# Kernel tuning notes

Measured on AMD Instinct MI355X. Metric: run time of the kernel, lower is better.

## Reference

```python
import jax, jax.numpy as jnp
import numpy as np

T, N_SAT, G_SAT, HID, IN = 256, 1024, 2048, 256, 32

def _make_sids(key):
    # per-timestep unique visible-satellite ids (matches dict-keyed state, no dup scatter)
    keys = jax.random.split(key, T)
    return jax.vmap(lambda k: jax.random.permutation(k, G_SAT)[:N_SAT])(keys).astype(jnp.int32)

def setup_inputs() -> dict:
    key = jax.random.key(0)
    ks = jax.random.split(key, 16)
    s = 0.05
    return {
        "x_rec": jax.random.normal(ks[0], (T, 1, IN), jnp.float32),
        "x_sat": jax.random.normal(ks[1], (T, N_SAT, IN), jnp.float32),
        "y_true": jax.random.normal(ks[2], (1, 2), jnp.float32),
        "W_rec": jax.random.normal(ks[3], (4, IN, HID), jnp.float32) * s,
        "b_rec": jax.random.normal(ks[4], (4, HID), jnp.float32) * s,
        "W_sat": jax.random.normal(ks[5], (4, IN, HID), jnp.float32) * s,
        "b_sat": jax.random.normal(ks[6], (4, HID), jnp.float32) * s,
        "s2r_lw": jax.random.normal(ks[7], (4, HID, HID), jnp.float32) * s,
        "s2r_lb": jax.random.normal(ks[8], (4, HID), jnp.float32) * s,
        "s2r_rw": jax.random.normal(ks[9], (4, HID, HID), jnp.float32) * s,
        "r2s_lw": jax.random.normal(ks[10], (4, HID, HID), jnp.float32) * s,
        "r2s_lb": jax.random.normal(ks[11], (4, HID), jnp.float32) * s,
        "r2s_rw": jax.random.normal(ks[12], (4, HID, HID), jnp.float32) * s,
        "W_out": jax.random.normal(ks[13], (HID, 2), jnp.float32) * s,
        "b_out": jax.random.normal(ks[14], (2,), jnp.float32) * s,
        "s_ids": _make_sids(ks[15]),
    }

def _gates(pre):
    # pre: [4, ..., HID] in gate order (i, f, c, o)
    return (jax.nn.sigmoid(pre[0]), jax.nn.sigmoid(pre[1]),
            jnp.tanh(pre[2]), jax.nn.sigmoid(pre[3]))

def reference(x_rec, x_sat, y_true, W_rec, b_rec, W_sat, b_sat,
              s2r_lw, s2r_lb, s2r_rw, r2s_lw, r2s_lb, r2s_rw,
              W_out, b_out, s_ids):
    hid = W_out.shape[0]

    def step(carry, inp):
        h_rec, c_rec, Hg, Cg = carry          # h_rec/c_rec: [hid]; Hg/Cg: [G, hid]
        xr, xs, sid = inp                      # xr: [1, in]; xs: [N, in]; sid: [N]
        h_sat = Hg[sid]                        # gather visible satellite states [N, hid]
        c_sat = Cg[sid]
        # per-gate input projections
        xr_p = jnp.einsum('i,gio->go', xr[0], W_rec) + b_rec          # [4, hid]
        xs_p = jnp.einsum('ni,gio->gno', xs, W_sat) + b_sat[:, None]  # [4, N, hid]
        # SAGEConv sat->rec: mean over all visible sats (star topology)
        mean_sat = jnp.mean(h_sat, axis=0)                            # [hid]
        conv_rec = (jnp.einsum('h,gho->go', mean_sat, s2r_lw) + s2r_lb
                    + jnp.einsum('h,gho->go', h_rec, s2r_rw))         # [4, hid]
        # SAGEConv rec->sat: each sat's sole neighbor is the receiver
        conv_sat = ((jnp.einsum('h,gho->go', h_rec, r2s_lw) + r2s_lb)[:, None, :]
                    + jnp.einsum('nh,gho->gno', h_sat, r2s_rw))       # [4, N, hid]
        i_r, f_r, t_r, o_r = _gates(xr_p + conv_rec)
        c_rec_n = f_r * c_rec + i_r * t_r
        h_rec_n = o_r * jnp.tanh(c_rec_n)
        i_s, f_s, t_s, o_s = _gates(xs_p + conv_sat)
        c_sat_n = f_s * c_sat + i_s * t_s
        h_sat_n = o_s * jnp.tanh(c_sat_n)
        Hg = Hg.at[sid].set(h_sat_n)
        Cg = Cg.at[sid].set(c_sat_n)
        return (h_rec_n, c_rec_n, Hg, Cg), None

    init = (jnp.zeros((hid,), x_rec.dtype), jnp.zeros((hid,), x_rec.dtype),
            jnp.zeros((G_SAT, hid), x_rec.dtype), jnp.zeros((G_SAT, hid), x_rec.dtype))
    (h_rec, _, _, _), _ = jax.lax.scan(step, init, (x_rec, x_sat, s_ids))
    pred = h_rec[None, :] @ W_out + b_out   # dropout is identity in eval mode
    return pred, y_true
```

## Files before the change

kernel.cpp:

```cpp
#include <hip/hip_runtime.h>
#include <cstddef>

#define T_STEPS  256
#define NSAT     1024
#define GSAT     2048
#define HID      256
#define IN_DIM   32
#define KTOT     288

typedef short  s16x8 __attribute__((ext_vector_type(8)));
typedef short  s16x4 __attribute__((ext_vector_type(4)));
typedef float  f32x4 __attribute__((ext_vector_type(4)));
typedef unsigned short ushort_t;

__device__ inline ushort_t f2bf(float f) {
    unsigned u = __builtin_bit_cast(unsigned, f);
    u += 0x7fffu + ((u >> 16) & 1u);
    return (ushort_t)(u >> 16);
}
__device__ inline float bf2f(ushort_t h) {
    unsigned u = ((unsigned)h) << 16;
    return __builtin_bit_cast(float, u);
}
__device__ inline float sigm(float x) { return 1.f / (1.f + __expf(-x)); }
__device__ inline float tanh_(float x) {
    float a = fabsf(x);
    float e = __expf(-2.f * a);
    float r = (1.f - e) / (1.f + e);
    return copysignf(r, x);
}

__global__ void k_zero(float* p, size_t n) {
    size_t i = (size_t)blockIdx.x * blockDim.x + threadIdx.x;
    size_t stride = (size_t)gridDim.x * blockDim.x;
    for (; i < n; i += stride) p[i] = 0.f;
}

__global__ void k_bconv(const float* __restrict__ r2s_rw,
                        const float* __restrict__ W_sat,
                        ushort_t* __restrict__ BsatT) {
    int c = blockIdx.x;
    int g = (c >> 3) & 3, o = (c >> 5) * 8 + (c & 7);
    for (int k = threadIdx.x; k < KTOT; k += 256) {
        float v = (k < 256) ? r2s_rw[((size_t)g * 256 + k) * 256 + o]
                            : W_sat[((size_t)g * 32 + (k - 256)) * 256 + o];
        BsatT[(size_t)c * KTOT + k] = f2bf(v);
    }
}

__global__ void k_rlw(const float* __restrict__ r2s_lw, ushort_t* __restrict__ rlw_bf) {
    int c = blockIdx.x;
    int g = (c >> 3) & 3, o = (c >> 5) * 8 + (c & 7);
    int h = threadIdx.x;
    rlw_bf[(size_t)c * 256 + h] = f2bf(r2s_lw[((size_t)g * 256 + h) * 256 + o]);
}

__global__ void k_biasC(const float* __restrict__ r2s_lb, const float* __restrict__ b_sat,
                        float* __restrict__ biasC) {
    int c = blockIdx.x * 256 + threadIdx.x;
    if (c < 1024) {
        int g = (c >> 3) & 3, o = (c >> 5) * 8 + (c & 7);
        biasC[c] = r2s_lb[g * 256 + o] + b_sat[g * 256 + o];
    }
}

__global__ void k_inv(const int* __restrict__ s_ids, ushort_t* __restrict__ pos_inv) {
    int t = blockIdx.x;
    for (int n = threadIdx.x; n < NSAT; n += 256)
        pos_inv[(size_t)t * GSAT + s_ids[(size_t)t * NSAT + n]] = (ushort_t)(n + 1);
}

__global__ void k_asrc(const int* __restrict__ s_ids, const ushort_t* __restrict__ pos_inv,
                       int* __restrict__ asrc) {
    int t = blockIdx.x;
    for (int n = threadIdx.x; n < NSAT; n += 256) {
        int j = s_ids[(size_t)t * NSAT + n];
        int e = 1024 + j;
        if (t > 0) {
            int p = (int)pos_inv[(size_t)(t - 1) * GSAT + j] - 1;
            if (p >= 0) e = p;
        }
        asrc[(size_t)t * NSAT + n] = e;
    }
}

__global__ void k_bits(const int* __restrict__ s_ids, const ushort_t* __restrict__ pos_inv,
                       unsigned* __restrict__ nxt_bits) {
    int t = blockIdx.x, w = threadIdx.x;
    unsigned bits = 0;
    if (t + 1 < T_STEPS) {
        for (int i = 0; i < 32; i++) {
            int j = s_ids[(size_t)t * NSAT + w * 32 + i];
            if (pos_inv[(size_t)(t + 1) * GSAT + j] > 0) bits |= (1u << i);
        }
    }
    nxt_bits[t * 32 + w] = bits;
}

__global__ void k_old(const int* __restrict__ s_ids, const ushort_t* __restrict__ pos_inv,
                      short* __restrict__ old_src, int* __restrict__ old_cnt) {
    int t = blockIdx.x;
    if (t + 1 >= T_STEPS) return;
    for (int n = threadIdx.x; n < NSAT; n += 256) {
        int j = s_ids[(size_t)(t + 1) * NSAT + n];
        if (pos_inv[(size_t)t * GSAT + j] == 0) {
            int slot = atomicAdd(&old_cnt[t], 1);
            short e = (short)(-(j + 1));
            if (t > 0) {
                int p = (int)pos_inv[(size_t)(t - 1) * GSAT + j] - 1;
                if (p >= 0) e = (short)p;
            }
            old_src[(size_t)t * NSAT + slot] = e;
        }
    }
}

__global__ void k_lv(const int* __restrict__ s_ids, const ushort_t* __restrict__ pos_inv,
                     int* __restrict__ lv, int* __restrict__ lv_cnt) {
    int t = blockIdx.x;
    if (t == 0) return;
    for (int n = threadIdx.x; n < NSAT; n += 256) {
        int j = s_ids[(size_t)(t - 1) * NSAT + n];
        if (pos_inv[(size_t)t * GSAT + j] == 0) {
            int slot = atomicAdd(&lv_cnt[t], 1);
            lv[(size_t)t * NSAT + slot] = (n << 16) | j;
        }
    }
}

__global__ void k_wtb(const float* __restrict__ in, ushort_t* __restrict__ outT) {
    __shared__ float tl[32][33];
    int g = blockIdx.z;
    int h0 = blockIdx.x * 32, o0 = blockIdx.y * 32;
    int lx = threadIdx.x & 31, ly = threadIdx.x >> 5;
#pragma unroll
    for (int i = 0; i < 32; i += 8)
        tl[ly + i][lx] = in[((size_t)g * 256 + h0 + ly + i) * 256 + o0 + lx];
    __syncthreads();
#pragma unroll
    for (int i = 0; i < 32; i += 8)
        outT[((size_t)g * 256 + o0 + ly + i) * 256 + h0 + lx] = f2bf(tl[lx][ly + i]);
}

__global__ void k_wrt(const float* __restrict__ W_rec, float* __restrict__ W_recT) {
    int idx = blockIdx.x * 256 + threadIdx.x;
    int g = idx >> 8, o = idx & 255;
#pragma unroll
    for (int i = 0; i < 32; i++)
        W_recT[(size_t)idx * 32 + i] = W_rec[((size_t)g * 32 + i) * 256 + o];
}

__launch_bounds__(256)
__global__ void k_step(int t,
    const float* __restrict__ x_rec, const float* __restrict__ x_sat,
    const float* __restrict__ b_rec, const float* __restrict__ s2r_lb,
    const int* __restrict__ asrc, const unsigned* __restrict__ nxt_bits,
    const short* __restrict__ old_src, const int* __restrict__ old_cnt,
    const int* __restrict__ lv, const int* __restrict__ lv_cnt,
    const ushort_t* __restrict__ BsatT, const ushort_t* __restrict__ rlw_bf,
    const float* __restrict__ biasC,
    const ushort_t* __restrict__ s2r_rwT, const ushort_t* __restrict__ s2r_lwT,
    const float* __restrict__ W_recT,
    float* __restrict__ meanN,
    float* __restrict__ oldpart,
    float* __restrict__ crec,
    float* __restrict__ pre_rec,
    ushort_t* __restrict__ Hg_bf, ushort_t* __restrict__ Cg_bf,
    const ushort_t* __restrict__ HnP, ushort_t* __restrict__ HnC,
    const ushort_t* __restrict__ CnP, ushort_t* __restrict__ CnC)
{
    const int b = blockIdx.x, tid = threadIdx.x;
    const float* preP  = pre_rec + ((t + 1) & 1) * 1024;
    const float* crecP = crec + (t & 1) * 256;

    if (b < 256) {
        const int by = b >> 5, bxc = b & 31;
        __shared__ ushort_t hr_bfs[256];
        __shared__ float    bias_s[32];
        __shared__ float    rl_s[32];
        __shared__ float    pre_s[128][33];

        const int w = tid >> 6, l = tid & 63;
        const int lr = l & 15, kb = (l >> 4) * 8;
        const int r0 = w * 32 + lr, r1 = r0 + 16;
        const int* asrc_t = asrc + (size_t)t * NSAT + by * 128;

        const int e0 = asrc_t[r0], e1 = asrc_t[r1];
        if (tid < 32) bias_s[tid] = biasC[bxc * 32 + tid];
        const int n_ep = tid >> 1, oi0_ep = (tid & 1) * 4;
        const int og0_ep = bxc * 8 + oi0_ep;
        const int en_ep = asrc_t[n_ep];
        const ushort_t* csrc = (en_ep < 1024) ? CnP + (size_t)en_ep * HID + og0_ep
                                              : Cg_bf + (size_t)(en_ep - 1024) * HID + og0_ep;
        s16x4 cold4 = *(const s16x4*)csrc;
        const int lv_m = lv_cnt[t];
        ushort_t pH[4], pC[4]; int pJ[4];
#pragma unroll
        for (int i = 0; i < 4; i++) {
            int k = b + i * 256;
            if (k < lv_m) {
                int pv = lv[(size_t)t * NSAT + k];
                int pos = pv >> 16; pJ[i] = pv & 0xffff;
                pH[i] = HnP[(size_t)pos * HID + tid];
                pC[i] = CnP[(size_t)pos * HID + tid];
            } else pJ[i] = -1;
        }
        {
            float h = 0.f;
            if (t > 0) {
                float pi = preP[tid], pf = preP[256 + tid], pc = preP[512 + tid], po = preP[768 + tid];
                float cp = (t >= 2) ? crecP[tid] : 0.f;
                float cn = sigm(pf) * cp + sigm(pi) * tanh_(pc);
                h = sigm(po) * tanh_(cn);
            }
            hr_bfs[tid] = f2bf(h);
        }

        const ushort_t* a0 = (e0 < 1024) ? HnP + (size_t)e0 * HID : Hg_bf + (size_t)(e0 - 1024) * HID;
        const ushort_t* a1 = (e1 < 1024) ? HnP + (size_t)e1 * HID : Hg_bf + (size_t)(e1 - 1024) * HID;
        const ushort_t* bp0 = BsatT + ((size_t)(bxc * 32 + lr)) * KTOT;
        const ushort_t* bp1 = bp0 + (size_t)16 * KTOT;
        f32x4 a00 = {0.f,0.f,0.f,0.f}, a01 = a00, a10 = a00, a11 = a00;
#pragma unroll
        for (int kc = 0; kc < 8; kc++) {
            int k0 = kc * 32 + kb;
            s16x8 af0 = *(const s16x8*)(a0 + k0);
            s16x8 af1 = *(const s16x8*)(a1 + k0);
            s16x8 bv0 = *(const s16x8*)(bp0 + k0);
            s16x8 bv1 = *(const s16x8*)(bp1 + k0);
            a00 = __builtin_amdgcn_mfma_f32_16x16x32_bf16(af0, bv0, a00, 0, 0, 0);
            a01 = __builtin_amdgcn_mfma_f32_16x16x32_bf16(af0, bv1, a01, 0, 0, 0);
            a10 = __builtin_amdgcn_mfma_f32_16x16x32_bf16(af1, bv0, a10, 0, 0, 0);
            a11 = __builtin_amdgcn_mfma_f32_16x16x32_bf16(af1, bv1, a11, 0, 0, 0);
        }
        {
            const float* ax0 = x_sat + ((size_t)t * NSAT + by * 128 + r0) * IN_DIM + kb;
            const float* ax1 = x_sat + ((size_t)t * NSAT + by * 128 + r1) * IN_DIM + kb;
            f32x4 x00 = *(const f32x4*)ax0, x01 = *(const f32x4*)(ax0 + 4);
            f32x4 x10 = *(const f32x4*)ax1, x11 = *(const f32x4*)(ax1 + 4);
            s16x8 af0, af1;
#pragma unroll
            for (int e = 0; e < 4; e++) {
                af0[e] = (short)f2bf(x00[e]); af0[4 + e] = (short)f2bf(x01[e]);
                af1[e] = (short)f2bf(x10[e]); af1[4 + e] = (short)f2bf(x11[e]);
            }
            int k0 = 256 + kb;
            s16x8 bv0 = *(const s16x8*)(bp0 + k0);
            s16x8 bv1 = *(const s16x8*)(bp1 + k0);
            a00 = __builtin_amdgcn_mfma_f32_16x16x32_bf16(af0, bv0, a00, 0, 0, 0);
            a01 = __builtin_amdgcn_mfma_f32_16x16x32_bf16(af0, bv1, a01, 0, 0, 0);
            a10 = __builtin_amdgcn_mfma_f32_16x16x32_bf16(af1, bv0, a10, 0, 0, 0);
            a11 = __builtin_amdgcn_mfma_f32_16x16x32_bf16(af1, bv1, a11, 0, 0, 0);
        }
#pragma unroll
        for (int rr = 0; rr < 4; rr++) {
            int ro = (l >> 4) * 4 + rr;
            pre_s[w * 32 + ro][lr]           = a00[rr];
            pre_s[w * 32 + ro][16 + lr]      = a01[rr];
            pre_s[w * 32 + 16 + ro][lr]      = a10[rr];
            pre_s[w * 32 + 16 + ro][16 + lr] = a11[rr];
        }
        __syncthreads();

        {
            int c = tid >> 3, sub = tid & 7;
            const ushort_t* wp = rlw_bf + ((size_t)(bxc * 32 + c)) * 256 + sub * 32;
            float acc = 0.f;
#pragma unroll
            for (int q = 0; q < 4; q++) {
                s16x8 wv = *(const s16x8*)(wp + q * 8);
#pragma unroll
                for (int e = 0; e < 8; e++)
                    acc += bf2f(hr_bfs[sub * 32 + q * 8 + e]) * bf2f((ushort_t)wv[e]);
            }
            acc += __shfl_down(acc, 4);
            acc += __shfl_down(acc, 2);
            acc += __shfl_down(acc, 1);
            if (sub == 0) rl_s[c] = acc + bias_s[c];
        }
        __syncthreads();

        {
            int n = n_ep, oi0 = oi0_ep, og0 = og0_ep;
            int gr = by * 128 + n;
            bool nxt = (t + 1 < T_STEPS) && ((nxt_bits[t * 32 + (gr >> 5)] >> (gr & 31)) & 1u);
            f32x4 hf; s16x4 cnew, hnew;
#pragma unroll
            for (int e = 0; e < 4; e++) {
                int oi = oi0 + e;
                float pi = pre_s[n][oi]      + rl_s[oi];
                float pf = pre_s[n][8 + oi]  + rl_s[8 + oi];
                float pc = pre_s[n][16 + oi] + rl_s[16 + oi];
                float po = pre_s[n][24 + oi] + rl_s[24 + oi];
                float ig = sigm(pi), fg = sigm(pf), tg = tanh_(pc), oo = sigm(po);
                float cn = fg * bf2f((ushort_t)cold4[e]) + ig * tg;
                float hn = oo * tanh_(cn);
                hf[e] = hn;
                cnew[e] = (short)f2bf(cn);
                hnew[e] = (short)f2bf(hn);
            }
            *(s16x4*)(CnC + (size_t)gr * HID + og0) = cnew;
            *(s16x4*)(HnC + (size_t)gr * HID + og0) = hnew;
#pragma unroll
            for (int e = 0; e < 4; e++) pre_s[n][oi0 + e] = nxt ? hf[e] : 0.f;
        }
        __syncthreads();
        if (t + 1 < T_STEPS && tid < 8) {
            float s = 0.f;
            for (int n = 0; n < 128; n++) s += pre_s[n][tid];
            meanN[((t + 1) & 1) * 2048 + by * 256 + bxc * 8 + tid] = s;
        }

#pragma unroll
        for (int i = 0; i < 4; i++) {
            if (pJ[i] >= 0) {
                Hg_bf[(size_t)pJ[i] * HID + tid] = pH[i];
                Cg_bf[(size_t)pJ[i] * HID + tid] = pC[i];
            }
        }
    } else {
        const int r = b - 256;
        __shared__ float mean_s[256], hr_s[256], xr_s[32];
        const int m_old = (t + 1 < T_STEPS) ? old_cnt[t] : 0;
        {
            float s = 0.f;
            const float* mp = meanN + (t & 1) * 2048;
#pragma unroll
            for (int p = 0; p < 8; p++) s += mp[p * 256 + tid];
            const float* op = oldpart + (t & 1) * 8192;
#pragma unroll 8
            for (int p = 0; p < 32; p++) s += op[p * 256 + tid];
            mean_s[tid] = s * (1.f / 1024.f);
        }
        {
            float h = 0.f, cn = 0.f;
            if (t > 0) {
                float pi = preP[tid], pf = preP[256 + tid], pc = preP[512 + tid], po = preP[768 + tid];
                float cp = (t >= 2) ? crecP[tid] : 0.f;
                cn = sigm(pf) * cp + sigm(pi) * tanh_(pc);
                h = sigm(po) * tanh_(cn);
            }
            hr_s[tid] = h;
            if (r == 0 && t > 0) crec[((t + 1) & 1) * 256 + tid] = cn;
        }
        if (tid < 32) xr_s[tid] = x_rec[(size_t)t * IN_DIM + tid];
        __syncthreads();
        float s_old = 0.f;
        {
            const short* osp = old_src + (size_t)t * NSAT;
#pragma unroll 2
            for (int k = r; k < m_old; k += 32) {
                int e = osp[k];
                const ushort_t* hp = (e >= 0) ? HnP + (size_t)e * HID
                                              : Hg_bf + (size_t)(-(e + 1)) * HID;
                s_old += bf2f(hp[tid]);
            }
        }
        {
            const int combo = tid >> 3, sub = tid & 7;
            const int g = combo >> 3, oo = combo & 7;
            const int o = r * 8 + oo;
            const ushort_t* rwp = s2r_rwT + ((size_t)(g * 256 + o)) * 256 + sub * 32;
            const ushort_t* lwp = s2r_lwT + ((size_t)(g * 256 + o)) * 256 + sub * 32;
            float part = 0.f;
#pragma unroll
            for (int q = 0; q < 4; q++) {
                s16x8 a = *(const s16x8*)(rwp + q * 8);
                s16x8 c = *(const s16x8*)(lwp + q * 8);
#pragma unroll
                for (int e = 0; e < 8; e++) {
                    int h = sub * 32 + q * 8 + e;
                    part += hr_s[h] * bf2f((ushort_t)a[e]) + mean_s[h] * bf2f((ushort_t)c[e]);
                }
            }
            {
                f32x4 wx = *(const f32x4*)(W_recT + ((size_t)(g * 256 + o)) * 32 + sub * 4);
#pragma unroll
                for (int e = 0; e < 4; e++) part += xr_s[sub * 4 + e] * wx[e];
            }
            part += __shfl_down(part, 4);
            part += __shfl_down(part, 2);
            part += __shfl_down(part, 1);
            if (sub == 0)
                pre_rec[(t & 1) * 1024 + g * 256 + o] =
                    part + b_rec[g * HID + o] + s2r_lb[g * HID + o];
        }
        if (t + 1 < T_STEPS)
            oldpart[((t + 1) & 1) * 8192 + r * 256 + tid] = s_old;
    }
}

__global__ void k_final(const float* __restrict__ pre_rec,
                        const float* __restrict__ crec,
                        const float* __restrict__ W_out,
                        const float* __restrict__ b_out,
                        const float* __restrict__ y_true,
                        float* __restrict__ out) {
    __shared__ float red[256];
    int o = threadIdx.x;
    const float* pre = pre_rec + ((T_STEPS - 1) & 1) * 1024;
    float pi = pre[o], pf = pre[256 + o], pc = pre[512 + o], po = pre[768 + o];
    float cp = crec[(T_STEPS & 1) * 256 + o];
    float cn = sigm(pf) * cp + sigm(pi) * tanh_(pc);
    float h = sigm(po) * tanh_(cn);
    for (int j = 0; j < 2; j++) {
        red[o] = h * W_out[o * 2 + j];
        __syncthreads();
        for (int s = 128; s > 0; s >>= 1) {
            if (o < s) red[o] += red[o + s];
            __syncthreads();
        }
        if (o == 0) out[j] = red[0] + b_out[j];
        __syncthreads();
    }
    if (o < 2) out[2 + o] = y_true[o];
}

extern "C" void kernel_launch(void* const* d_in, const int* in_sizes, int n_in,
                              void* d_out, int out_size, void* d_ws, size_t ws_size,
                              hipStream_t stream) {
    (void)in_sizes; (void)n_in; (void)out_size; (void)ws_size;
    const float* x_rec  = (const float*)d_in[0];
    const float* x_sat  = (const float*)d_in[1];
    const float* y_true = (const float*)d_in[2];
    const float* W_rec  = (const float*)d_in[3];
    const float* b_rec  = (const float*)d_in[4];
    const float* W_sat  = (const float*)d_in[5];
    const float* b_sat  = (const float*)d_in[6];
    const float* s2r_lw = (const float*)d_in[7];
    const float* s2r_lb = (const float*)d_in[8];
    const float* s2r_rw = (const float*)d_in[9];
    const float* r2s_lw = (const float*)d_in[10];
    const float* r2s_lb = (const float*)d_in[11];
    const float* r2s_rw = (const float*)d_in[12];
    const float* W_out  = (const float*)d_in[13];
    const float* b_out  = (const float*)d_in[14];
    const int*   s_ids  = (const int*)d_in[15];

    float* ws = (float*)d_ws;
    size_t off = 0;
    float*    meanN    = ws + off;              off += 4096;
    float*    oldpart  = ws + off;              off += 16384;
    float*    crec     = ws + off;              off += 512;
    float*    pre_rec  = ws + off;              off += 2048;
    int*      old_cnt  = (int*)(ws + off);      off += 256;
    int*      lv_cnt   = (int*)(ws + off);      off += 256;
    ushort_t* Hg_bf    = (ushort_t*)(ws + off); off += 262144;
    ushort_t* Cg_bf    = (ushort_t*)(ws + off); off += 262144;
    ushort_t* pos_inv  = (ushort_t*)(ws + off); off += 262144;
    int*      asrc     = (int*)(ws + off);      off += 262144;
    unsigned* nxt_bits = (unsigned*)(ws + off); off += 8192;
    short*    old_src  = (short*)(ws + off);    off += 131072;
    int*      lv       = (int*)(ws + off);      off += 262144;
    ushort_t* HnewA    = (ushort_t*)(ws + off); off += 131072;
    ushort_t* HnewB    = (ushort_t*)(ws + off); off += 131072;
    ushort_t* CnewA    = (ushort_t*)(ws + off); off += 131072;
    ushort_t* CnewB    = (ushort_t*)(ws + off); off += 131072;
    ushort_t* BsatT    = (ushort_t*)(ws + off); off += 147456;
    ushort_t* rlw_bf   = (ushort_t*)(ws + off); off += 131072;
    float*    biasC    = ws + off;              off += 1024;
    ushort_t* s2r_rwT  = (ushort_t*)(ws + off); off += 131072;
    ushort_t* s2r_lwT  = (ushort_t*)(ws + off); off += 131072;
    float*    W_recT   = ws + off;              off += 32768;

    const size_t zcount = 4096 + 16384 + 512 + 2048 + 256 + 256
                        + 262144 + 262144 + 262144;
    hipLaunchKernelGGL(k_zero, dim3(2048), dim3(256), 0, stream, ws, zcount);
    hipLaunchKernelGGL(k_inv, dim3(T_STEPS), dim3(256), 0, stream, s_ids, pos_inv);
    hipLaunchKernelGGL(k_asrc, dim3(T_STEPS), dim3(256), 0, stream, s_ids, pos_inv, asrc);
    hipLaunchKernelGGL(k_bits, dim3(T_STEPS), dim3(32), 0, stream, s_ids, pos_inv, nxt_bits);
    hipLaunchKernelGGL(k_old, dim3(T_STEPS), dim3(256), 0, stream, s_ids, pos_inv, old_src, old_cnt);
    hipLaunchKernelGGL(k_lv, dim3(T_STEPS), dim3(256), 0, stream, s_ids, pos_inv, lv, lv_cnt);
    hipLaunchKernelGGL(k_bconv, dim3(1024), dim3(256), 0, stream, r2s_rw, W_sat, BsatT);
    hipLaunchKernelGGL(k_rlw, dim3(1024), dim3(256), 0, stream, r2s_lw, rlw_bf);
    hipLaunchKernelGGL(k_biasC, dim3(4), dim3(256), 0, stream, r2s_lb, b_sat, biasC);
    hipLaunchKernelGGL(k_wtb, dim3(8, 8, 4), dim3(256), 0, stream, s2r_rw, s2r_rwT);
    hipLaunchKernelGGL(k_wtb, dim3(8, 8, 4), dim3(256), 0, stream, s2r_lw, s2r_lwT);
    hipLaunchKernelGGL(k_wrt, dim3(4), dim3(256), 0, stream, W_rec, W_recT);

    for (int t = 0; t < T_STEPS; t++) {
        const ushort_t* HnP = (t & 1) ? HnewA : HnewB;
        ushort_t*       HnC = (t & 1) ? HnewB : HnewA;
        const ushort_t* CnP = (t & 1) ? CnewA : CnewB;
        ushort_t*       CnC = (t & 1) ? CnewB : CnewA;
        hipLaunchKernelGGL(k_step, dim3(288), dim3(256), 0, stream,
                           t, x_rec, x_sat, b_rec, s2r_lb,
                           asrc, nxt_bits, old_src, old_cnt, lv, lv_cnt,
                           BsatT, rlw_bf, biasC,
                           s2r_rwT, s2r_lwT, W_recT,
                           meanN, oldpart, crec, pre_rec,
                           Hg_bf, Cg_bf, HnP, HnC, CnP, CnC);
    }
    hipLaunchKernelGGL(k_final, dim3(1), dim3(256), 0, stream,
                       pre_rec, crec, W_out, b_out, y_true, (float*)d_out);
}
```

Baseline: 3.378 ms.

## Precompute receiver-to-satellite projection in receiver blocks one step ahead

Each satellite block used to recompute the previous receiver hidden state and then do its own 256-long dot product with r2s_lw. Now the 32 receiver blocks compute the new receiver h for their 8 outputs at the end of the step and write partial products into a double-buffered rlpart array. The next step's satellite blocks only sum 32 partials, which removes one barrier and the redundant gate and dot-product work. The change also merges four index-preprocessing kernels into one and replaces the serial 128-row mean loop with a shuffle reduction. The cost is extra global traffic for rlpart and more serial work at the end of the receiver blocks.

```diff
diff --git a/kernel.cpp b/kernel.cpp
--- a/kernel.cpp
+++ b/kernel.cpp
@@ -48,11 +48,12 @@
     }
 }
 
-__global__ void k_rlw(const float* __restrict__ r2s_lw, ushort_t* __restrict__ rlw_bf) {
-    int c = blockIdx.x;
-    int g = (c >> 3) & 3, o = (c >> 5) * 8 + (c & 7);
-    int h = threadIdx.x;
-    rlw_bf[(size_t)c * 256 + h] = f2bf(r2s_lw[((size_t)g * 256 + h) * 256 + o]);
+__global__ void k_rlw2(const float* __restrict__ r2s_lw, ushort_t* __restrict__ rlwT2) {
+    int h = blockIdx.x;
+    for (int c = threadIdx.x; c < 1024; c += 256) {
+        int g = (c >> 3) & 3, o = (c >> 5) * 8 + (c & 7);
+        rlwT2[(size_t)h * 1024 + c] = f2bf(r2s_lw[((size_t)g * 256 + h) * 256 + o]);
+    }
 }
 
 __global__ void k_biasC(const float* __restrict__ r2s_lb, const float* __restrict__ b_sat,
@@ -70,10 +71,12 @@
         pos_inv[(size_t)t * GSAT + s_ids[(size_t)t * NSAT + n]] = (ushort_t)(n + 1);
 }
 
-__global__ void k_asrc(const int* __restrict__ s_ids, const ushort_t* __restrict__ pos_inv,
-                       int* __restrict__ asrc) {
-    int t = blockIdx.x;
-    for (int n = threadIdx.x; n < NSAT; n += 256) {
+__global__ void k_idx(const int* __restrict__ s_ids, const ushort_t* __restrict__ pos_inv,
+                      int* __restrict__ asrc, unsigned* __restrict__ nxt_bits,
+                      short* __restrict__ old_src, int* __restrict__ old_cnt,
+                      int* __restrict__ lv, int* __restrict__ lv_cnt) {
+    int t = blockIdx.x, tid = threadIdx.x;
+    for (int n = tid; n < NSAT; n += 256) {
         int j = s_ids[(size_t)t * NSAT + n];
         int e = 1024 + j;
         if (t > 0) {
@@ -82,48 +85,37 @@
         }
         asrc[(size_t)t * NSAT + n] = e;
     }
-}
-
-__global__ void k_bits(const int* __restrict__ s_ids, const ushort_t* __restrict__ pos_inv,
-                       unsigned* __restrict__ nxt_bits) {
-    int t = blockIdx.x, w = threadIdx.x;
-    unsigned bits = 0;
+    if (tid < 32) {
+        unsigned bits = 0;
+        if (t + 1 < T_STEPS) {
+            for (int i = 0; i < 32; i++) {
+                int j = s_ids[(size_t)t * NSAT + tid * 32 + i];
+                if (pos_inv[(size_t)(t + 1) * GSAT + j] > 0) bits |= (1u << i);
+            }
+        }
+        nxt_bits[t * 32 + tid] = bits;
+    }
     if (t + 1 < T_STEPS) {
-        for (int i = 0; i < 32; i++) {
-            int j = s_ids[(size_t)t * NSAT + w * 32 + i];
-            if (pos_inv[(size_t)(t + 1) * GSAT + j] > 0) bits |= (1u << i);
-        }
-    }
-    nxt_bits[t * 32 + w] = bits;
-}
-
-__global__ void k_old(const int* __restrict__ s_ids, const ushort_t* __restrict__ pos_inv,
-                      short* __restrict__ old_src, int* __restrict__ old_cnt) {
-    int t = blockIdx.x;
-    if (t + 1 >= T_STEPS) return;
-    for (int n = threadIdx.x; n < NSAT; n += 256) {
-        int j = s_ids[(size_t)(t + 1) * NSAT + n];
-        if (pos_inv[(size_t)t * GSAT + j] == 0) {
-            int slot = atomicAdd(&old_cnt[t], 1);
-            short e = (short)(-(j + 1));
-            if (t > 0) {
-                int p = (int)pos_inv[(size_t)(t - 1) * GSAT + j] - 1;
-                if (p >= 0) e = (short)p;
-            }
-            old_src[(size_t)t * NSAT + slot] = e;
-        }
-    }
-}
-
-__global__ void k_lv(const int* __restrict__ s_ids, const ushort_t* __restrict__ pos_inv,
-                     int* __restrict__ lv, int* __restrict__ lv_cnt) {
-    int t = blockIdx.x;
-    if (t == 0) return;
-    for (int n = threadIdx.x; n < NSAT; n += 256) {
-        int j = s_ids[(size_t)(t - 1) * NSAT + n];
-        if (pos_inv[(size_t)t * GSAT + j] == 0) {
-            int slot = atomicAdd(&lv_cnt[t], 1);
-            lv[(size_t)t * NSAT + slot] = (n << 16) | j;
+        for (int n = tid; n < NSAT; n += 256) {
+            int j = s_ids[(size_t)(t + 1) * NSAT + n];
+            if (pos_inv[(size_t)t * GSAT + j] == 0) {
+                int slot = atomicAdd(&old_cnt[t], 1);
+                short e = (short)(-(j + 1));
+                if (t > 0) {
+                    int p = (int)pos_inv[(size_t)(t - 1) * GSAT + j] - 1;
+                    if (p >= 0) e = (short)p;
+                }
+                old_src[(size_t)t * NSAT + slot] = e;
+            }
+        }
+    }
+    if (t > 0) {
+        for (int n = tid; n < NSAT; n += 256) {
+            int j = s_ids[(size_t)(t - 1) * NSAT + n];
+            if (pos_inv[(size_t)t * GSAT + j] == 0) {
+                int slot = atomicAdd(&lv_cnt[t], 1);
+                lv[(size_t)t * NSAT + slot] = (n << 16) | j;
+            }
         }
     }
 }
@@ -157,7 +149,7 @@
     const int* __restrict__ asrc, const unsigned* __restrict__ nxt_bits,
     const short* __restrict__ old_src, const int* __restrict__ old_cnt,
     const int* __restrict__ lv, const int* __restrict__ lv_cnt,
-    const ushort_t* __restrict__ BsatT, const ushort_t* __restrict__ rlw_bf,
+    const ushort_t* __restrict__ BsatT, const ushort_t* __restrict__ rlwT2,
     const float* __restrict__ biasC,
     const ushort_t* __restrict__ s2r_rwT, const ushort_t* __restrict__ s2r_lwT,
     const float* __restrict__ W_recT,
@@ -165,6 +157,7 @@
     float* __restrict__ oldpart,
     float* __restrict__ crec,
     float* __restrict__ pre_rec,
+    float* __restrict__ rlpart,
     ushort_t* __restrict__ Hg_bf, ushort_t* __restrict__ Cg_bf,
     const ushort_t* __restrict__ HnP, ushort_t* __restrict__ HnC,
     const ushort_t* __restrict__ CnP, ushort_t* __restrict__ CnC)
@@ -175,10 +168,8 @@
 
     if (b < 256) {
         const int by = b >> 5, bxc = b & 31;
-        __shared__ ushort_t hr_bfs[256];
-        __shared__ float    bias_s[32];
-        __shared__ float    rl_s[32];
-        __shared__ float    pre_s[128][33];
+        __shared__ float rl_s[32];
+        __shared__ float pre_s[128][33];
 
         const int w = tid >> 6, l = tid & 63;
         const int lr = l & 15, kb = (l >> 4) * 8;
@@ -186,13 +177,15 @@
         const int* asrc_t = asrc + (size_t)t * NSAT + by * 128;
 
         const int e0 = asrc_t[r0], e1 = asrc_t[r1];
-        if (tid < 32) bias_s[tid] = biasC[bxc * 32 + tid];
         const int n_ep = tid >> 1, oi0_ep = (tid & 1) * 4;
         const int og0_ep = bxc * 8 + oi0_ep;
         const int en_ep = asrc_t[n_ep];
         const ushort_t* csrc = (en_ep < 1024) ? CnP + (size_t)en_ep * HID + og0_ep
                                               : Cg_bf + (size_t)(en_ep - 1024) * HID + og0_ep;
         s16x4 cold4 = *(const s16x4*)csrc;
+        const int gr_ep = by * 128 + n_ep;
+        const bool nxt = (t + 1 < T_STEPS) &&
+                         ((nxt_bits[t * 32 + (gr_ep >> 5)] >> (gr_ep & 31)) & 1u);
         const int lv_m = lv_cnt[t];
         ushort_t pH[4], pC[4]; int pJ[4];
 #pragma unroll
@@ -204,16 +197,6 @@
                 pH[i] = HnP[(size_t)pos * HID + tid];
                 pC[i] = CnP[(size_t)pos * HID + tid];
             } else pJ[i] = -1;
-        }
-        {
-            float h = 0.f;
-            if (t > 0) {
-                float pi = preP[tid], pf = preP[256 + tid], pc = preP[512 + tid], po = preP[768 + tid];
-                float cp = (t >= 2) ? crecP[tid] : 0.f;
-                float cn = sigm(pf) * cp + sigm(pi) * tanh_(pc);
-                h = sigm(po) * tanh_(cn);
-            }
-            hr_bfs[tid] = f2bf(h);
         }
 
         const ushort_t* a0 = (e0 < 1024) ? HnP + (size_t)e0 * HID : Hg_bf + (size_t)(e0 - 1024) * HID;
@@ -252,6 +235,19 @@
             a10 = __builtin_amdgcn_mfma_f32_16x16x32_bf16(af1, bv0, a10, 0, 0, 0);
             a11 = __builtin_amdgcn_mfma_f32_16x16x32_bf16(af1, bv1, a11, 0, 0, 0);
         }
+
+        {
+            int c = tid >> 3, sub = tid & 7;
+            const float* rp = rlpart + (size_t)(t & 1) * 32768 + bxc * 32 + c;
+            float part = rp[(size_t)(sub * 4 + 0) * 1024]
+                       + rp[(size_t)(sub * 4 + 1) * 1024]
+                       + rp[(size_t)(sub * 4 + 2) * 1024]
+                       + rp[(size_t)(sub * 4 + 3) * 1024];
+            part += __shfl_down(part, 4, 8);
+            part += __shfl_down(part, 2, 8);
+            part += __shfl_down(part, 1, 8);
+            if (sub == 0) rl_s[c] = part + biasC[bxc * 32 + c];
+        }
 #pragma unroll
         for (int rr = 0; rr < 4; rr++) {
             int ro = (l >> 4) * 4 + rr;
@@ -263,27 +259,7 @@
         __syncthreads();
 
         {
-            int c = tid >> 3, sub = tid & 7;
-            const ushort_t* wp = rlw_bf + ((size_t)(bxc * 32 + c)) * 256 + sub * 32;
-            float acc = 0.f;
-#pragma unroll
-            for (int q = 0; q < 4; q++) {
-                s16x8 wv = *(const s16x8*)(wp + q * 8);
-#pragma unroll
-                for (int e = 0; e < 8; e++)
-                    acc += bf2f(hr_bfs[sub * 32 + q * 8 + e]) * bf2f((ushort_t)wv[e]);
-            }
-            acc += __shfl_down(acc, 4);
-            acc += __shfl_down(acc, 2);
-            acc += __shfl_down(acc, 1);
-            if (sub == 0) rl_s[c] = acc + bias_s[c];
-        }
-        __syncthreads();
-
-        {
             int n = n_ep, oi0 = oi0_ep, og0 = og0_ep;
-            int gr = by * 128 + n;
-            bool nxt = (t + 1 < T_STEPS) && ((nxt_bits[t * 32 + (gr >> 5)] >> (gr & 31)) & 1u);
             f32x4 hf; s16x4 cnew, hnew;
 #pragma unroll
             for (int e = 0; e < 4; e++) {
@@ -299,16 +275,23 @@
                 cnew[e] = (short)f2bf(cn);
                 hnew[e] = (short)f2bf(hn);
             }
-            *(s16x4*)(CnC + (size_t)gr * HID + og0) = cnew;
-            *(s16x4*)(HnC + (size_t)gr * HID + og0) = hnew;
-#pragma unroll
-            for (int e = 0; e < 4; e++) pre_s[n][oi0 + e] = nxt ? hf[e] : 0.f;
-        }
-        __syncthreads();
-        if (t + 1 < T_STEPS && tid < 8) {
-            float s = 0.f;
-            for (int n = 0; n < 128; n++) s += pre_s[n][tid];
-            meanN[((t + 1) & 1) * 2048 + by * 256 + bxc * 8 + tid] = s;
+            *(s16x4*)(CnC + (size_t)gr_ep * HID + og0) = cnew;
+            *(s16x4*)(HnC + (size_t)gr_ep * HID + og0) = hnew;
+#pragma unroll
+            for (int e = 0; e < 4; e++) pre_s[n_ep][oi0 + e] = nxt ? hf[e] : 0.f;
+        }
+        __syncthreads();
+        if (t + 1 < T_STEPS) {
+            int c = tid >> 5, lane = tid & 31;
+            float s = pre_s[lane][c] + pre_s[lane + 32][c]
+                    + pre_s[lane + 64][c] + pre_s[lane + 96][c];
+            s += __shfl_down(s, 16, 32);
+            s += __shfl_down(s, 8, 32);
+            s += __shfl_down(s, 4, 32);
+            s += __shfl_down(s, 2, 32);
+            s += __shfl_down(s, 1, 32);
+            if (lane == 0)
+                meanN[((t + 1) & 1) * 2048 + by * 256 + bxc * 8 + c] = s;
         }
 
 #pragma unroll
@@ -320,7 +303,7 @@
         }
     } else {
         const int r = b - 256;
-        __shared__ float mean_s[256], hr_s[256], xr_s[32];
+        __shared__ float mean_s[256], hr_s[256], xr_s[32], pre4[4][8], hn_s[8];
         const int m_old = (t + 1 < T_STEPS) ? old_cnt[t] : 0;
         {
             float s = 0.f;
@@ -332,16 +315,17 @@
             for (int p = 0; p < 32; p++) s += op[p * 256 + tid];
             mean_s[tid] = s * (1.f / 1024.f);
         }
-        {
-            float h = 0.f, cn = 0.f;
+        float cn_prev = 0.f;
+        {
+            float h = 0.f;
             if (t > 0) {
                 float pi = preP[tid], pf = preP[256 + tid], pc = preP[512 + tid], po = preP[768 + tid];
                 float cp = (t >= 2) ? crecP[tid] : 0.f;
-                cn = sigm(pf) * cp + sigm(pi) * tanh_(pc);
-                h = sigm(po) * tanh_(cn);
+                cn_prev = sigm(pf) * cp + sigm(pi) * tanh_(pc);
+                h = sigm(po) * tanh_(cn_prev);
             }
             hr_s[tid] = h;
-            if (r == 0 && t > 0) crec[((t + 1) & 1) * 256 + tid] = cn;
+            if (r == 0 && t > 0) crec[((t + 1) & 1) * 256 + tid] = cn_prev;
         }
         if (tid < 32) xr_s[tid] = x_rec[(size_t)t * IN_DIM + tid];
         __syncthreads();
@@ -381,12 +365,37 @@
             part += __shfl_down(part, 4);
             part += __shfl_down(part, 2);
             part += __shfl_down(part, 1);
-            if (sub == 0)
-                pre_rec[(t & 1) * 1024 + g * 256 + o] =
-                    part + b_rec[g * HID + o] + s2r_lb[g * HID + o];
+            if (sub == 0) {
+                float pv = part + b_rec[g * HID + o] + s2r_lb[g * HID + o];
+                pre_rec[(t & 1) * 1024 + g * 256 + o] = pv;
+                pre4[g][oo] = pv;
+            }
         }
         if (t + 1 < T_STEPS)
             oldpart[((t + 1) & 1) * 8192 + r * 256 + tid] = s_old;
+        __syncthreads();
+        if (tid >= r * 8 && tid < r * 8 + 8) {
+            int oo = tid - r * 8;
+            float pi = pre4[0][oo], pf = pre4[1][oo], pc = pre4[2][oo], po = pre4[3][oo];
+            float cp = (t > 0) ? cn_prev : 0.f;
+            float cnn = sigm(pf) * cp + sigm(pi) * tanh_(pc);
+            hn_s[oo] = sigm(po) * tanh_(cnn);
+        }
+        __syncthreads();
+        {
+            float acc0 = 0.f, acc1 = 0.f, acc2 = 0.f, acc3 = 0.f;
+#pragma unroll
+            for (int k8 = 0; k8 < 8; k8++) {
+                float hv = hn_s[k8];
+                s16x4 wv = *(const s16x4*)(rlwT2 + (size_t)(r * 8 + k8) * 1024 + tid * 4);
+                acc0 += hv * bf2f((ushort_t)wv[0]);
+                acc1 += hv * bf2f((ushort_t)wv[1]);
+                acc2 += hv * bf2f((ushort_t)wv[2]);
+                acc3 += hv * bf2f((ushort_t)wv[3]);
+            }
+            float* dst = rlpart + (size_t)((t + 1) & 1) * 32768 + r * 1024 + tid * 4;
+            dst[0] = acc0; dst[1] = acc1; dst[2] = acc2; dst[3] = acc3;
+        }
     }
 }
 
@@ -445,6 +454,7 @@
     float*    pre_rec  = ws + off;              off += 2048;
     int*      old_cnt  = (int*)(ws + off);      off += 256;
     int*      lv_cnt   = (int*)(ws + off);      off += 256;
+    float*    rlpart   = ws + off;              off += 65536;
     ushort_t* Hg_bf    = (ushort_t*)(ws + off); off += 262144;
     ushort_t* Cg_bf    = (ushort_t*)(ws + off); off += 262144;
     ushort_t* pos_inv  = (ushort_t*)(ws + off); off += 262144;
@@ -457,22 +467,20 @@
     ushort_t* CnewA    = (ushort_t*)(ws + off); off += 131072;
     ushort_t* CnewB    = (ushort_t*)(ws + off); off += 131072;
     ushort_t* BsatT    = (ushort_t*)(ws + off); off += 147456;
-    ushort_t* rlw_bf   = (ushort_t*)(ws + off); off += 131072;
+    ushort_t* rlwT2    = (ushort_t*)(ws + off); off += 131072;
     float*    biasC    = ws + off;              off += 1024;
     ushort_t* s2r_rwT  = (ushort_t*)(ws + off); off += 131072;
     ushort_t* s2r_lwT  = (ushort_t*)(ws + off); off += 131072;
     float*    W_recT   = ws + off;              off += 32768;
 
-    const size_t zcount = 4096 + 16384 + 512 + 2048 + 256 + 256
+    const size_t zcount = 4096 + 16384 + 512 + 2048 + 256 + 256 + 65536
                         + 262144 + 262144 + 262144;
     hipLaunchKernelGGL(k_zero, dim3(2048), dim3(256), 0, stream, ws, zcount);
     hipLaunchKernelGGL(k_inv, dim3(T_STEPS), dim3(256), 0, stream, s_ids, pos_inv);
-    hipLaunchKernelGGL(k_asrc, dim3(T_STEPS), dim3(256), 0, stream, s_ids, pos_inv, asrc);
-    hipLaunchKernelGGL(k_bits, dim3(T_STEPS), dim3(32), 0, stream, s_ids, pos_inv, nxt_bits);
-    hipLaunchKernelGGL(k_old, dim3(T_STEPS), dim3(256), 0, stream, s_ids, pos_inv, old_src, old_cnt);
-    hipLaunchKernelGGL(k_lv, dim3(T_STEPS), dim3(256), 0, stream, s_ids, pos_inv, lv, lv_cnt);
+    hipLaunchKernelGGL(k_idx, dim3(T_STEPS), dim3(256), 0, stream, s_ids, pos_inv,
+                       asrc, nxt_bits, old_src, old_cnt, lv, lv_cnt);
     hipLaunchKernelGGL(k_bconv, dim3(1024), dim3(256), 0, stream, r2s_rw, W_sat, BsatT);
-    hipLaunchKernelGGL(k_rlw, dim3(1024), dim3(256), 0, stream, r2s_lw, rlw_bf);
+    hipLaunchKernelGGL(k_rlw2, dim3(256), dim3(256), 0, stream, r2s_lw, rlwT2);
     hipLaunchKernelGGL(k_biasC, dim3(4), dim3(256), 0, stream, r2s_lb, b_sat, biasC);
     hipLaunchKernelGGL(k_wtb, dim3(8, 8, 4), dim3(256), 0, stream, s2r_rw, s2r_rwT);
     hipLaunchKernelGGL(k_wtb, dim3(8, 8, 4), dim3(256), 0, stream, s2r_lw, s2r_lwT);
@@ -486,9 +494,9 @@
         hipLaunchKernelGGL(k_step, dim3(288), dim3(256), 0, stream,
                            t, x_rec, x_sat, b_rec, s2r_lb,
                            asrc, nxt_bits, old_src, old_cnt, lv, lv_cnt,
-                           BsatT, rlw_bf, biasC,
+                           BsatT, rlwT2, biasC,
                            s2r_rwT, s2r_lwT, W_recT,
-                           meanN, oldpart, crec, pre_rec,
+                           meanN, oldpart, crec, pre_rec, rlpart,
                            Hg_bf, Cg_bf, HnP, HnC, CnP, CnC);
     }
     hipLaunchKernelGGL(k_final, dim3(1), dim3(256), 0, stream,
```

Result: slower. 3.615 ms (+7.0%).
